# Optimization experiments

Hardware: AMD Instinct MI355X
Metric: run time of the kernel (lower is better)

The kernel has to match this reference:

```python
import jax, jax.numpy as jnp
import numpy as np

B, M, S = 256, 32, 16          # batch, measures, steps per measure
IN, H, O = 512, 1024, 128      # input_dim, hidden_dim, output_dim


def _lstm(x, Wih, Whh, b):
    """PyTorch-convention LSTM (gates i,f,g,o), zero init state.
    x: [B, T, D] -> hidden trace [B, T, H]."""
    bsz = x.shape[0]
    h_dim = Whh.shape[1]
    # precompute input projections for all timesteps (one big GEMM)
    xg = jnp.einsum('btd,gd->btg', x, Wih) + b  # [B, T, 4H]

    def step(carry, xt):
        h, c = carry
        g = xt + h @ Whh.T
        i, f, gg, o = jnp.split(g, 4, axis=-1)
        c = jax.nn.sigmoid(f) * c + jax.nn.sigmoid(i) * jnp.tanh(gg)
        h = jax.nn.sigmoid(o) * jnp.tanh(c)
        return (h, c), h

    h0 = jnp.zeros((bsz, h_dim), x.dtype)
    (_, _), hs = jax.lax.scan(step, (h0, h0), jnp.swapaxes(xg, 0, 1))
    return jnp.swapaxes(hs, 0, 1)  # [B, T, H]


def setup_inputs() -> dict:
    key = jax.random.key(0)
    ks = jax.random.split(key, 10)
    sc = 0.02
    return {
        'latent': jax.random.normal(ks[0], (B, M, IN), jnp.float32),
        'inputs': jax.random.uniform(ks[1], (B, M, S, O), jnp.float32),
        'mWih': jax.random.normal(ks[2], (4 * H, IN), jnp.float32) * sc,
        'mWhh': jax.random.normal(ks[3], (4 * H, H), jnp.float32) * sc,
        'mb':   jax.random.normal(ks[4], (4 * H,), jnp.float32) * sc,
        'bWih': jax.random.normal(ks[5], (4 * H, H + O), jnp.float32) * sc,
        'bWhh': jax.random.normal(ks[6], (4 * H, H), jnp.float32) * sc,
        'bb':   jax.random.normal(ks[7], (4 * H,), jnp.float32) * sc,
        'linW': jax.random.normal(ks[8], (O, H), jnp.float32) * sc,
        'linb': jax.random.normal(ks[9], (O,), jnp.float32) * sc,
    }


def reference(latent, inputs, mWih, mWhh, mb, bWih, bWhh, bb, linW, linb):
    # measure-level LSTM + tanh -> per-measure latent codes [B, M, H]
    lat = jnp.tanh(_lstm(latent, mWih, mWhh, mb))
    # repeat each measure latent across its S beat steps -> [B, M*S, H]
    lat_rep = jnp.repeat(lat, S, axis=1)
    # beat-level LSTM runs over the full flattened sequence (hidden state
    # carries across measures exactly as in the torch loop)
    x = jnp.concatenate([lat_rep, inputs.reshape(B, M * S, O)], axis=-1)
    h = _lstm(x, bWih, bWhh, bb)              # [B, M*S, H]
    return jnp.tanh(h) @ linW.T + linb        # [B, M*S, O]
```

## Files before the change

### kernel.cpp

```cpp
#include <hip/hip_runtime.h>
#include <stdint.h>

typedef short s16x8 __attribute__((ext_vector_type(8)));
typedef float f32x4 __attribute__((ext_vector_type(4)));
typedef unsigned short u16;
typedef unsigned int u32;
typedef unsigned long long u64;

#define DEV static __device__ __forceinline__
#define SCOPE_AGENT __HIP_MEMORY_SCOPE_AGENT

DEV u16 f2bf(float f) {
  unsigned u = __float_as_uint(f);
  u = (u + 0x7FFFu + ((u >> 16) & 1u)) >> 16;
  return (u16)u;
}
DEV float sigf(float x) { return 1.0f / (1.0f + __expf(-x)); }
DEV float tanh_(float x) { float e = __expf(2.0f * x); return 1.0f - 2.0f / (e + 1.0f); }
DEV f32x4 MFMA(s16x8 a, s16x8 b, f32x4 c) {
  return __builtin_amdgcn_mfma_f32_16x16x32_bf16(a, b, c, 0, 0, 0);
}
DEV void cstore32(u32* p, u32 v) {
  __hip_atomic_store(p, v, __ATOMIC_RELAXED, SCOPE_AGENT);
}

constexpr int Bz = 256, INz = 512, Hz = 1024, Oz = 128;
constexpr int G4 = 4096;
constexpr int TB = 512;
constexpr int BM = 8192;

constexpr size_t OFF_XG   = 0;
constexpr size_t OFF_LATB = OFF_XG   + (size_t)BM * G4 * 4;
constexpr size_t OFF_INPB = OFF_LATB + (size_t)BM * INz * 2;
constexpr size_t OFF_MWIH = OFF_INPB + (size_t)Bz * TB * Oz * 2;
constexpr size_t OFF_MWHH = OFF_MWIH + (size_t)G4 * INz * 2;
constexpr size_t OFF_BWA  = OFF_MWHH + (size_t)G4 * Hz * 2;
constexpr size_t OFF_BWB  = OFF_BWA  + (size_t)G4 * Hz * 2;
constexpr size_t OFF_BWHH = OFF_BWB  + (size_t)G4 * Oz * 2;
constexpr size_t OFF_LINW = OFF_BWHH + (size_t)G4 * Hz * 2;
constexpr size_t OFF_LAT  = OFF_LINW + (size_t)Oz * Hz * 2;
constexpr size_t OFF_HM   = OFF_LAT  + (size_t)BM * Hz * 2;
constexpr size_t OFF_HB   = OFF_HM   + (size_t)2 * Bz * Hz * 2;
constexpr size_t OFF_RING = OFF_HB   + (size_t)2 * Bz * Hz * 2;
constexpr size_t OFF_CTR  = OFF_RING + (size_t)32 * Bz * Hz * 2;

__global__ __launch_bounds__(256) void prep_kernel(
    char* __restrict__ ws, const float* __restrict__ latent,
    const float* __restrict__ inputs, const float* __restrict__ mWih,
    const float* __restrict__ mWhh, const float* __restrict__ bWih,
    const float* __restrict__ bWhh, const float* __restrict__ linW)
{
  size_t i = (size_t)blockIdx.x * 256 + threadIdx.x;
  const size_t n0 = (size_t)BM * INz;
  const size_t n1 = (size_t)Bz * TB * Oz;
  const size_t n2 = (size_t)G4 * INz;
  const size_t n3 = (size_t)G4 * Hz;
  const size_t n4 = (size_t)G4 * (Hz + Oz);
  const size_t n5 = (size_t)G4 * Hz;
  const size_t n6 = (size_t)Oz * Hz;
  const size_t n7 = (size_t)2 * Bz * Hz;
  const size_t n8 = (size_t)2 * Bz * Hz;
  const size_t n9 = 512;
  if (i < n0) { ((u16*)(ws + OFF_LATB))[i] = f2bf(latent[i]); return; } i -= n0;
  if (i < n1) { ((u16*)(ws + OFF_INPB))[i] = f2bf(inputs[i]); return; } i -= n1;
  if (i < n2) { ((u16*)(ws + OFF_MWIH))[i] = f2bf(mWih[i]);   return; } i -= n2;
  if (i < n3) { ((u16*)(ws + OFF_MWHH))[i] = f2bf(mWhh[i]);   return; } i -= n3;
  if (i < n4) {
    size_t r = i / 1152, c = i - r * 1152;
    float v = bWih[i];
    if (c < 1024) ((u16*)(ws + OFF_BWA))[r * 1024 + c] = f2bf(v);
    else          ((u16*)(ws + OFF_BWB))[r * 128 + (c - 1024)] = f2bf(v);
    return;
  } i -= n4;
  if (i < n5) { ((u16*)(ws + OFF_BWHH))[i] = f2bf(bWhh[i]);   return; } i -= n5;
  if (i < n6) { ((u16*)(ws + OFF_LINW))[i] = f2bf(linW[i]);   return; } i -= n6;
  if (i < n7) { ((u16*)(ws + OFF_HM))[i] = 0; return; } i -= n7;
  if (i < n8) { ((u16*)(ws + OFF_HB))[i] = 0; return; } i -= n8;
  if (i < n9) { ((unsigned*)(ws + OFF_CTR))[i] = 0; return; }
}

__global__ __launch_bounds__(256) void gemm_bt_bias(
    const u16* __restrict__ A, const u16* __restrict__ Bw,
    const float* __restrict__ bias, float* __restrict__ C, int K, int Ndim)
{
  __shared__ u16 As[128 * 40];
  __shared__ u16 Bs[128 * 40];
  const int bx = blockIdx.x & 63;
  const int by = blockIdx.x >> 6;
  const int m0 = bx * 128, n0 = by * 128;
  const int tid = threadIdx.x, lane = tid & 63, wave = tid >> 6;
  const int quad = lane >> 4, l15 = lane & 15;
  const int wm = wave & 1, wn = wave >> 1;
  const int srow = tid >> 1, shalf = tid & 1;

  f32x4 acc[4][4];
  #pragma unroll
  for (int mi = 0; mi < 4; ++mi)
    #pragma unroll
    for (int ni = 0; ni < 4; ++ni) { f32x4 z = {0.f,0.f,0.f,0.f}; acc[mi][ni] = z; }

  const int KC = K >> 5;
  for (int kc = 0; kc < KC; ++kc) {
    const size_t ka = (size_t)(m0 + srow) * K + kc * 32 + shalf * 16;
    s16x8 va0 = *(const s16x8*)(A + ka);
    s16x8 va1 = *(const s16x8*)(A + ka + 8);
    const size_t kb = (size_t)(n0 + srow) * K + kc * 32 + shalf * 16;
    s16x8 vb0 = *(const s16x8*)(Bw + kb);
    s16x8 vb1 = *(const s16x8*)(Bw + kb + 8);
    __syncthreads();
    *(s16x8*)(As + srow * 40 + shalf * 16)     = va0;
    *(s16x8*)(As + srow * 40 + shalf * 16 + 8) = va1;
    *(s16x8*)(Bs + srow * 40 + shalf * 16)     = vb0;
    *(s16x8*)(Bs + srow * 40 + shalf * 16 + 8) = vb1;
    __syncthreads();
    s16x8 af[4], bf[4];
    #pragma unroll
    for (int mi = 0; mi < 4; ++mi)
      af[mi] = *(const s16x8*)(As + (wm * 64 + mi * 16 + l15) * 40 + quad * 8);
    #pragma unroll
    for (int ni = 0; ni < 4; ++ni)
      bf[ni] = *(const s16x8*)(Bs + (wn * 64 + ni * 16 + l15) * 40 + quad * 8);
    #pragma unroll
    for (int mi = 0; mi < 4; ++mi)
      #pragma unroll
      for (int ni = 0; ni < 4; ++ni)
        acc[mi][ni] = MFMA(af[mi], bf[ni], acc[mi][ni]);
  }
  #pragma unroll
  for (int mi = 0; mi < 4; ++mi)
    #pragma unroll
    for (int ni = 0; ni < 4; ++ni) {
      const int col = n0 + wn * 64 + ni * 16 + l15;
      const float bs = bias[col];
      #pragma unroll
      for (int r = 0; r < 4; ++r) {
        const int row = m0 + wm * 64 + mi * 16 + quad * 4 + r;
        C[(size_t)row * Ndim + col] = acc[mi][ni][r] + bs;
      }
    }
}

DEV void oproj_step(const u16* __restrict__ aux, const u16* __restrict__ linW,
                    const float* __restrict__ linb, float* __restrict__ dout,
                    int bt, int t0, int wave, int quad, int l15)
{
  const u16* base = aux + (size_t)(t0 & 31) * 262144 + ((size_t)bt << 16);
  const u16* orp = base + (((quad << 6) + (wave << 4) + l15) << 3);
  const u16* lp[8];
  #pragma unroll
  for (int nt = 0; nt < 8; ++nt)
    lp[nt] = linW + (((size_t)(nt << 4) + l15) << 10) + (quad << 3);
  f32x4 oacc[8];
  #pragma unroll
  for (int nt = 0; nt < 8; ++nt) { f32x4 z = {0.f,0.f,0.f,0.f}; oacc[nt] = z; }
  s16x8 opf[4];
  #pragma unroll
  for (int g = 0; g < 4; ++g)
    opf[g] = *(const s16x8*)(orp + (g << 11));
  #pragma unroll
  for (int kc = 0; kc < 32; ++kc) {
    const s16x8 a = opf[kc & 3];
    #pragma unroll
    for (int nt = 0; nt < 8; ++nt) {
      s16x8 b = *(const s16x8*)(lp[nt] + (kc << 5));
      oacc[nt] = MFMA(a, b, oacc[nt]);
    }
    if (kc < 28)
      opf[kc & 3] = *(const s16x8*)(orp + ((size_t)(kc + 4) << 11));
  }
  #pragma unroll
  for (int nt = 0; nt < 8; ++nt) {
    const int col = (nt << 4) + l15;
    const float bs = linb[col];
    #pragma unroll
    for (int r = 0; r < 4; ++r) {
      const int bg2 = (bt << 6) + (wave << 4) + (quad << 2) + r;
      dout[((size_t)bg2 * 512 + t0) * 128 + col] = oacc[nt][r] + bs;
    }
  }
}

template<bool BEAT>
__global__ __launch_bounds__(256, 2) void lstm_rec(
    const u16* __restrict__ Whh,
    const float* __restrict__ xg,
    const u16* __restrict__ WihB,
    const u16* __restrict__ inp,
    const u16* __restrict__ linW,
    const float* __restrict__ linb,
    u16* __restrict__ hbuf0, u16* __restrict__ hbuf1,
    u16* __restrict__ aux,
    float* __restrict__ dout,
    unsigned* __restrict__ ctr)
{
  extern __shared__ char smem[];
  u16* sW = (u16*)smem;
  float* sEx = (float*)(smem + 66048);
  u32* sSt = (u32*)(smem + 66048 + 8448);

  const int blk = blockIdx.x;
  const int bt = blk >> 7, ht = blk & 127;
  const int tid = threadIdx.x;
  const int wave = tid >> 6, lane = tid & 63;
  const int quad = lane >> 4, l15 = lane & 15;

  unsigned* const arr = ctr + (bt << 6);
  unsigned* const flg = arr + 32;

  for (int c = tid; c < 4096; c += 256) {
    const int rr = c >> 7;
    const int cc = (c & 127) << 3;
    const int gr = ((rr >> 3) << 10) + (ht << 3) + (rr & 7);
    *(s16x8*)(sW + rr * 1032 + cc) = *(const s16x8*)(Whh + ((size_t)gr << 10) + cc);
  }
  __syncthreads();

  const int batch_l = tid & 63, dgrp = tid >> 6;
  const int b_g = (bt << 6) + batch_l;
  float cst[2] = {0.f, 0.f};
  float xgv[4][2];

  const int T = BEAT ? 512 : 32;
  const u16* hbufs[2] = {hbuf0, hbuf1};

  for (int t = 0; t < T; ++t) {
    const u16* hp = hbufs[t & 1];
    u16* hn = const_cast<u16*>(hbufs[(t + 1) & 1]);

    if (!BEAT || (t & 15) == 0) {
      const int mrow = BEAT ? (t >> 4) : t;
      const float* xr = xg + (size_t)(b_g * 32 + mrow) * 4096 + (ht << 3) + (dgrp << 1);
      #pragma unroll
      for (int g = 0; g < 4; ++g)
        #pragma unroll
        for (int j = 0; j < 2; ++j) xgv[g][j] = xr[g * 1024 + j];
    }

    f32x4 acc[2];
    { f32x4 z = {0.f,0.f,0.f,0.f}; acc[0] = z; acc[1] = z; }

    if (BEAT) {
      #pragma unroll
      for (int kc = 0; kc < 4; ++kc) {
        const int k = (kc << 5) + (quad << 3);
        const int r0 = (((l15 >> 3) << 10) + (ht << 3) + (l15 & 7));
        s16x8 bfr0 = *(const s16x8*)(WihB + (size_t)r0 * 128 + k);
        s16x8 bfr1 = *(const s16x8*)(WihB + (size_t)(r0 + 2048) * 128 + k);
        s16x8 afr = *(const s16x8*)(inp + ((size_t)((bt << 6) + (wave << 4) + l15) * 512 + t) * 128 + k);
        acc[0] = MFMA(afr, bfr0, acc[0]);
        acc[1] = MFMA(afr, bfr1, acc[1]);
      }
    }

    if (t) {
      if (tid == 0) {
        while (__hip_atomic_load(flg, __ATOMIC_RELAXED, SCOPE_AGENT) < (unsigned)t)
          __builtin_amdgcn_s_sleep(2);
        (void)__hip_atomic_load(flg, __ATOMIC_ACQUIRE, SCOPE_AGENT);
      }
      __syncthreads();
      __atomic_signal_fence(__ATOMIC_SEQ_CST);
    }

    if (BEAT && t && (t & 15) == 0 && ht < 16)
      oproj_step(aux, linW, linb, dout, bt, t - 16 + ht, wave, quad, l15);

    {
      const u16* hbase = hp + ((size_t)bt << 16);
      const u16* ap = hbase + (((quad << 6) + (wave << 4) + l15) << 3);
      s16x8 pf[8];
      #pragma unroll
      for (int g = 0; g < 8; ++g)
        pf[g] = *(const s16x8*)(ap + (g << 11));

      const u16* sB0 = sW + (l15) * 1032 + (quad << 3);
      const u16* sB1 = sW + (16 + l15) * 1032 + (quad << 3);
      #pragma unroll
      for (int kc = 0; kc < 32; ++kc) {
        s16x8 bfr0 = *(const s16x8*)(sB0 + (kc << 5));
        s16x8 bfr1 = *(const s16x8*)(sB1 + (kc << 5));
        acc[0] = MFMA(pf[kc & 7], bfr0, acc[0]);
        acc[1] = MFMA(pf[kc & 7], bfr1, acc[1]);
        if (kc < 24)
          pf[kc & 7] = *(const s16x8*)(ap + ((size_t)(kc + 8) << 11));
      }
    }

    #pragma unroll
    for (int c = 0; c < 2; ++c)
      #pragma unroll
      for (int r = 0; r < 4; ++r)
        sEx[((wave << 4) + (quad << 2) + r) * 33 + (c << 4) + l15] = acc[c][r];
    __syncthreads();

    float hv[2], tv[2];
    {
      const int bo = batch_l * 33;
      #pragma unroll
      for (int j = 0; j < 2; ++j) {
        const int d = (dgrp << 1) + j;
        const float pi  = sEx[bo + d]        + xgv[0][j];
        const float pf_ = sEx[bo + 8 + d]    + xgv[1][j];
        const float pg  = sEx[bo + 16 + d]   + xgv[2][j];
        const float po  = sEx[bo + 24 + d]   + xgv[3][j];
        const float iv = sigf(pi), fv = sigf(pf_), gv = tanh_(pg), ov = sigf(po);
        cst[j] = fv * cst[j] + iv * gv;
        hv[j] = ov * tanh_(cst[j]);
        tv[j] = tanh_(hv[j]);
      }
    }
    const u32 hpk = (u32)f2bf(hv[0]) | ((u32)f2bf(hv[1]) << 16);
    const u32 tpk = (u32)f2bf(tv[0]) | ((u32)f2bf(tv[1]) << 16);

    sSt[batch_l * 4 + dgrp] = hpk;
    if (BEAT) sSt[256 + batch_l * 4 + dgrp] = tpk;
    __syncthreads();
    {
      u32* hdst = (u32*)hn + (((size_t)(bt << 7) + ht) << 8);
      cstore32(hdst + tid, sSt[tid]);
      if (BEAT) {
        u32* rdst = (u32*)aux + (size_t)(t & 31) * 131072 + (((size_t)(bt << 7) + ht) << 8);
        cstore32(rdst + tid, sSt[256 + tid]);
      } else {
        cstore32((u32*)(aux + ((size_t)(b_g * 32 + t) << 10) + (ht << 3) + (dgrp << 1)), tpk);
      }
    }

    __syncthreads();
    if (tid == 0) {
      const unsigned old = __hip_atomic_fetch_add(arr, 1u, __ATOMIC_RELAXED, SCOPE_AGENT);
      if (old == (unsigned)((t + 1) * 128 - 1))
        __hip_atomic_store(flg, (unsigned)(t + 1), __ATOMIC_RELAXED, SCOPE_AGENT);
    }
  }

  if (BEAT) {
    if (tid == 0) {
      while (__hip_atomic_load(flg, __ATOMIC_RELAXED, SCOPE_AGENT) < (unsigned)T)
        __builtin_amdgcn_s_sleep(2);
      (void)__hip_atomic_load(flg, __ATOMIC_ACQUIRE, SCOPE_AGENT);
    }
    __syncthreads();
    __atomic_signal_fence(__ATOMIC_SEQ_CST);
    if (ht < 16)
      oproj_step(aux, linW, linb, dout, bt, T - 16 + ht, wave, quad, l15);
  }
}

extern "C" void kernel_launch(void* const* d_in, const int* in_sizes, int n_in,
                              void* d_out, int out_size, void* d_ws, size_t ws_size,
                              hipStream_t stream) {
  (void)in_sizes; (void)n_in; (void)out_size; (void)ws_size;
  const float* latent = (const float*)d_in[0];
  const float* inputs = (const float*)d_in[1];
  const float* mWih   = (const float*)d_in[2];
  const float* mWhh   = (const float*)d_in[3];
  const float* mb     = (const float*)d_in[4];
  const float* bWih   = (const float*)d_in[5];
  const float* bWhh   = (const float*)d_in[6];
  const float* bb     = (const float*)d_in[7];
  const float* linW   = (const float*)d_in[8];
  const float* linb   = (const float*)d_in[9];
  char* ws = (char*)d_ws;

  float* xg    = (float*)(ws + OFF_XG);
  u16* latb    = (u16*)(ws + OFF_LATB);
  u16* inpb    = (u16*)(ws + OFF_INPB);
  u16* mwihb   = (u16*)(ws + OFF_MWIH);
  u16* mwhhb   = (u16*)(ws + OFF_MWHH);
  u16* bwab    = (u16*)(ws + OFF_BWA);
  u16* bwbb    = (u16*)(ws + OFF_BWB);
  u16* bwhhb   = (u16*)(ws + OFF_BWHH);
  u16* linwb   = (u16*)(ws + OFF_LINW);
  u16* latT    = (u16*)(ws + OFF_LAT);
  u16* hm      = (u16*)(ws + OFF_HM);
  u16* hb      = (u16*)(ws + OFF_HB);
  u16* ring    = (u16*)(ws + OFF_RING);
  unsigned* cs = (unsigned*)(ws + OFF_CTR);

  constexpr unsigned SMEM = 66048 + 8448 + 2048;
  hipFuncSetAttribute((const void*)(&lstm_rec<false>),
                      hipFuncAttributeMaxDynamicSharedMemorySize, (int)SMEM);
  hipFuncSetAttribute((const void*)(&lstm_rec<true>),
                      hipFuncAttributeMaxDynamicSharedMemorySize, (int)SMEM);

  {
    const size_t total = 37356032ull;
    const int blocks = (int)((total + 255) / 256);
    prep_kernel<<<blocks, 256, 0, stream>>>(ws, latent, inputs, mWih, mWhh, bWih, bWhh, linW);
  }
  gemm_bt_bias<<<2048, 256, 0, stream>>>(latb, mwihb, mb, xg, 512, 4096);

  {
    const u16* a_whh = mwhhb; const float* a_xg = xg; const u16* a_wib = bwbb;
    const u16* a_inp = inpb;  const u16* a_lw = linwb; const float* a_lb = linb;
    u16* a_h0 = hm; u16* a_h1 = hm + Bz * Hz; u16* a_aux = latT;
    float* a_do = (float*)d_out; unsigned* a_ct = cs;
    void* margs[] = {&a_whh, &a_xg, &a_wib, &a_inp, &a_lw, &a_lb,
                     &a_h0, &a_h1, &a_aux, &a_do, &a_ct};
    hipError_t e = hipLaunchCooperativeKernel((const void*)(&lstm_rec<false>),
                                              dim3(512), dim3(256), margs, SMEM, stream);
    if (e != hipSuccess) {
      lstm_rec<false><<<512, 256, SMEM, stream>>>(mwhhb, xg, bwbb, inpb, linwb, linb,
                                                  hm, hm + Bz * Hz, latT,
                                                  (float*)d_out, cs);
    }
  }
  gemm_bt_bias<<<2048, 256, 0, stream>>>(latT, bwab, bb, xg, 1024, 4096);

  {
    const u16* a_whh = bwhhb; const float* a_xg = xg; const u16* a_wib = bwbb;
    const u16* a_inp = inpb;  const u16* a_lw = linwb; const float* a_lb = linb;
    u16* a_h0 = hb; u16* a_h1 = hb + Bz * Hz; u16* a_aux = ring;
    float* a_do = (float*)d_out; unsigned* a_ct = cs + 256;
    void* bargs[] = {&a_whh, &a_xg, &a_wib, &a_inp, &a_lw, &a_lb,
                     &a_h0, &a_h1, &a_aux, &a_do, &a_ct};
    hipError_t e = hipLaunchCooperativeKernel((const void*)(&lstm_rec<true>),
                                              dim3(512), dim3(256), bargs, SMEM, stream);
    if (e != hipSuccess) {
      lstm_rec<true><<<512, 256, SMEM, stream>>>(bwhhb, xg, bwbb, inpb, linwb, linb,
                                                 hb, hb + Bz * Hz, ring,
                                                 (float*)d_out, cs + 256);
    }
  }
}
```

Measured before the change: 9.340 ms.

## Replace atomic-counter barrier with per-block flag slots; defer output projection

Replaces the fetch-add arrival counter plus release flag with per-block step slots. Each block stores its step number and one wave polls all 128 slots with a vote, which removes the serialized atomic RMW and the extra hop through a last-arriver flag. It also moves the periodic output-projection step off the barrier's critical path to two steps later, so it overlaps with the next recurrence. The cost is more polling traffic (128 loads per waiter) and a larger counter region.

```diff
diff --git a/kernel.cpp b/kernel.cpp
--- a/kernel.cpp
+++ b/kernel.cpp
@@ -22,6 +22,9 @@
 }
 DEV void cstore32(u32* p, u32 v) {
   __hip_atomic_store(p, v, __ATOMIC_RELAXED, SCOPE_AGENT);
+}
+DEV u32 cload32(const u32* p) {
+  return __hip_atomic_load((u32*)p, __ATOMIC_RELAXED, SCOPE_AGENT);
 }
 
 constexpr int Bz = 256, INz = 512, Hz = 1024, Oz = 128;
@@ -60,7 +63,7 @@
   const size_t n6 = (size_t)Oz * Hz;
   const size_t n7 = (size_t)2 * Bz * Hz;
   const size_t n8 = (size_t)2 * Bz * Hz;
-  const size_t n9 = 512;
+  const size_t n9 = 1024;
   if (i < n0) { ((u16*)(ws + OFF_LATB))[i] = f2bf(latent[i]); return; } i -= n0;
   if (i < n1) { ((u16*)(ws + OFF_INPB))[i] = f2bf(inputs[i]); return; } i -= n1;
   if (i < n2) { ((u16*)(ws + OFF_MWIH))[i] = f2bf(mWih[i]);   return; } i -= n2;
@@ -204,8 +207,7 @@
   const int wave = tid >> 6, lane = tid & 63;
   const int quad = lane >> 4, l15 = lane & 15;
 
-  unsigned* const arr = ctr + (bt << 6);
-  unsigned* const flg = arr + 32;
+  unsigned* const slots = ctr + (bt << 7);
 
   for (int c = tid; c < 4096; c += 256) {
     const int rr = c >> 7;
@@ -226,6 +228,9 @@
   for (int t = 0; t < T; ++t) {
     const u16* hp = hbufs[t & 1];
     u16* hn = const_cast<u16*>(hbufs[(t + 1) & 1]);
+
+    if (BEAT && (t & 15) == 2 && t > 16 && ht < 16)
+      oproj_step(aux, linW, linb, dout, bt, t - 18 + ht, wave, quad, l15);
 
     if (!BEAT || (t & 15) == 0) {
       const int mrow = BEAT ? (t >> 4) : t;
@@ -253,17 +258,20 @@
     }
 
     if (t) {
-      if (tid == 0) {
-        while (__hip_atomic_load(flg, __ATOMIC_RELAXED, SCOPE_AGENT) < (unsigned)t)
+      const unsigned tgt = (unsigned)t;
+      if (tid < 64) {
+        for (;;) {
+          unsigned a = cload32(slots + tid);
+          unsigned b = cload32(slots + 64 + tid);
+          if (__all(a >= tgt && b >= tgt)) break;
           __builtin_amdgcn_s_sleep(2);
-        (void)__hip_atomic_load(flg, __ATOMIC_ACQUIRE, SCOPE_AGENT);
+        }
+        if (tid == 0)
+          (void)__hip_atomic_load(slots, __ATOMIC_ACQUIRE, SCOPE_AGENT);
       }
       __syncthreads();
       __atomic_signal_fence(__ATOMIC_SEQ_CST);
     }
-
-    if (BEAT && t && (t & 15) == 0 && ht < 16)
-      oproj_step(aux, linW, linb, dout, bt, t - 16 + ht, wave, quad, l15);
 
     {
       const u16* hbase = hp + ((size_t)bt << 16);
@@ -327,18 +335,21 @@
     }
 
     __syncthreads();
-    if (tid == 0) {
-      const unsigned old = __hip_atomic_fetch_add(arr, 1u, __ATOMIC_RELAXED, SCOPE_AGENT);
-      if (old == (unsigned)((t + 1) * 128 - 1))
-        __hip_atomic_store(flg, (unsigned)(t + 1), __ATOMIC_RELAXED, SCOPE_AGENT);
-    }
+    if (tid == 0)
+      cstore32(slots + ht, (unsigned)(t + 1));
   }
 
   if (BEAT) {
-    if (tid == 0) {
-      while (__hip_atomic_load(flg, __ATOMIC_RELAXED, SCOPE_AGENT) < (unsigned)T)
+    const unsigned tgt = (unsigned)T;
+    if (tid < 64) {
+      for (;;) {
+        unsigned a = cload32(slots + tid);
+        unsigned b = cload32(slots + 64 + tid);
+        if (__all(a >= tgt && b >= tgt)) break;
         __builtin_amdgcn_s_sleep(2);
-      (void)__hip_atomic_load(flg, __ATOMIC_ACQUIRE, SCOPE_AGENT);
+      }
+      if (tid == 0)
+        (void)__hip_atomic_load(slots, __ATOMIC_ACQUIRE, SCOPE_AGENT);
     }
     __syncthreads();
     __atomic_signal_fence(__ATOMIC_SEQ_CST);
@@ -385,7 +396,7 @@
                       hipFuncAttributeMaxDynamicSharedMemorySize, (int)SMEM);
 
   {
-    const size_t total = 37356032ull;
+    const size_t total = 37356544ull;
     const int blocks = (int)((total + 255) / 256);
     prep_kernel<<<blocks, 256, 0, stream>>>(ws, latent, inputs, mWih, mWhh, bWih, bWhh, linW);
   }
@@ -412,7 +423,7 @@
     const u16* a_whh = bwhhb; const float* a_xg = xg; const u16* a_wib = bwbb;
     const u16* a_inp = inpb;  const u16* a_lw = linwb; const float* a_lb = linb;
     u16* a_h0 = hb; u16* a_h1 = hb + Bz * Hz; u16* a_aux = ring;
-    float* a_do = (float*)d_out; unsigned* a_ct = cs + 256;
+    float* a_do = (float*)d_out; unsigned* a_ct = cs + 512;
     void* bargs[] = {&a_whh, &a_xg, &a_wib, &a_inp, &a_lw, &a_lb,
                      &a_h0, &a_h1, &a_aux, &a_do, &a_ct};
     hipError_t e = hipLaunchCooperativeKernel((const void*)(&lstm_rec<true>),
@@ -420,7 +431,7 @@
     if (e != hipSuccess) {
       lstm_rec<true><<<512, 256, SMEM, stream>>>(bwhhb, xg, bwbb, inpb, linwb, linb,
                                                  hb, hb + Bz * Hz, ring,
-                                                 (float*)d_out, cs + 256);
-    }
-  }
-}
+                                                 (float*)d_out, cs + 512);
+    }
+  }
+}
```

Result: faster. 8.447 ms (-9.6%).
